# Performance work log

Measured on AMD Instinct MI355X. Metric: run time of the kernel, lower is better.

The kernel has to match this reference:

```python
import jax, jax.numpy as jnp
import numpy as np

N = 100000
E = 600000
G = 8
HID = 128
HEADS = 4
C = HID // HEADS  # 32


def setup_inputs() -> dict:
    key = jax.random.key(0)
    ks = jax.random.split(key, 32)
    s = 0.05
    node_numeric = jax.random.normal(ks[0], (N, 8), jnp.float32)
    node_cat0 = jax.random.randint(ks[1], (N,), 0, 32)
    node_cat1 = jax.random.randint(ks[2], (N,), 0, 64)
    edge_numeric = jax.random.normal(ks[3], (E, 4), jnp.float32)
    edge_cat0 = jax.random.randint(ks[4], (E,), 0, 16)
    edge_cat1 = jax.random.randint(ks[5], (E,), 0, 100)
    src = jax.random.randint(ks[6], (E,), 0, N)
    dst = jax.random.randint(ks[7], (E,), 0, N)
    dst = jnp.where(dst == src, (dst + 1) % N, dst)  # GATConv removes self-loops before adding its own
    edge_index = jnp.stack([src, dst])
    batch = jnp.sort(jax.random.randint(ks[8], (N,), 0, G))
    recipe = jax.random.normal(ks[9], (G, 16), jnp.float32)
    return dict(
        node_numeric=node_numeric, node_cat0=node_cat0, node_cat1=node_cat1,
        edge_numeric=edge_numeric, edge_cat0=edge_cat0, edge_cat1=edge_cat1,
        edge_index=edge_index, batch=batch, recipe=recipe,
        emb_node0=jax.random.normal(ks[10], (32, 6), jnp.float32) * s,
        emb_node1=jax.random.normal(ks[11], (64, 8), jnp.float32) * s,
        emb_edge0=jax.random.normal(ks[12], (16, 4), jnp.float32) * s,
        emb_edge1=jax.random.normal(ks[13], (100, 10), jnp.float32) * s,
        W_in=jax.random.normal(ks[14], (38, HID), jnp.float32) * s,
        b_in=jnp.zeros((HID,), jnp.float32),
        W_edge=jax.random.normal(ks[15], (18, HID), jnp.float32) * s,
        b_edge=jnp.zeros((HID,), jnp.float32),
        gat_lin=jax.random.normal(ks[16], (3, HID, HID), jnp.float32) * s,
        gat_lin_edge=jax.random.normal(ks[17], (3, HID, HID), jnp.float32) * s,
        att_src=jax.random.normal(ks[18], (3, HEADS, C), jnp.float32) * s,
        att_dst=jax.random.normal(ks[19], (3, HEADS, C), jnp.float32) * s,
        att_edge=jax.random.normal(ks[20], (3, HEADS, C), jnp.float32) * s,
        gat_bias=jnp.zeros((3, HID), jnp.float32),
        W_r1=jax.random.normal(ks[21], (HID, HID), jnp.float32) * s,
        b_r1=jnp.zeros((HID,), jnp.float32),
        W_r2=jax.random.normal(ks[22], (HID, 1), jnp.float32) * s,
        b_r2=jnp.zeros((1,), jnp.float32),
    )


def _segment_softmax(logits, seg, num):
    m = jax.ops.segment_max(logits, seg, num_segments=num)
    ex = jnp.exp(logits - m[seg])
    s = jax.ops.segment_sum(ex, seg, num_segments=num)
    return ex / s[seg]


def _forward(node_numeric, edge_numeric, recipe,
             emb_node0, emb_node1, emb_edge0, emb_edge1,
             W_in, b_in, W_edge, b_edge,
             gat_lin, gat_lin_edge, att_src, att_dst, att_edge, gat_bias,
             W_r1, b_r1, W_r2, b_r2,
             node_cat0, node_cat1, edge_cat0, edge_cat1, edge_index, batch):
    n = node_numeric.shape[0]
    src, dst = edge_index[0], edge_index[1]
    # node encoding: numeric + categorical embeddings + broadcast recipe
    h = jnp.concatenate([node_numeric, emb_node0[node_cat0], emb_node1[node_cat1], recipe[batch]], axis=1)
    h = jax.nn.relu(h @ W_in + b_in)
    # edge encoding (shared across GAT layers)
    e = jnp.concatenate([edge_numeric, emb_edge0[edge_cat0], emb_edge1[edge_cat1]], axis=1)
    e = e @ W_edge + b_edge
    # self-loops with fill_value='mean': per-dst mean of incoming edge_attr
    cnt = jax.ops.segment_sum(jnp.ones((e.shape[0],), e.dtype), dst, num_segments=n)
    loop = jax.ops.segment_sum(e, dst, num_segments=n) / jnp.maximum(cnt, 1.0)[:, None]
    ar = jnp.arange(n)
    src_a = jnp.concatenate([src, ar])
    dst_a = jnp.concatenate([dst, ar])
    e_a = jnp.concatenate([e, loop], axis=0)  # [E+N, HID]
    for l in range(gat_lin.shape[0]):
        x = (h @ gat_lin[l]).reshape(n, HEADS, C)          # shared lin_src/lin_dst
        ee = (e_a @ gat_lin_edge[l]).reshape(-1, HEADS, C)
        a_s = jnp.sum(x * att_src[l], axis=-1)   # [N, HEADS]
        a_d = jnp.sum(x * att_dst[l], axis=-1)
        a_e = jnp.sum(ee * att_edge[l], axis=-1)  # [E+N, HEADS]
        logits = jax.nn.leaky_relu(a_s[src_a] + a_d[dst_a] + a_e, negative_slope=0.2)
        alpha = _segment_softmax(logits, dst_a, n)  # segment softmax over dst
        out = jax.ops.segment_sum(x[src_a] * alpha[:, :, None], dst_a, num_segments=n)
        h = jax.nn.relu(out.reshape(n, HID) + gat_bias[l])  # dropout off (eval)
    g = jax.ops.segment_sum(h, batch, num_segments=G)  # global_add_pool
    g = jax.nn.relu(g @ W_r1 + b_r1)
    return g @ W_r2 + b_r2  # [G, 1]


def reference(node_numeric, node_cat0, node_cat1, edge_numeric, edge_cat0, edge_cat1,
              edge_index, batch, recipe,
              emb_node0, emb_node1, emb_edge0, emb_edge1,
              W_in, b_in, W_edge, b_edge,
              gat_lin, gat_lin_edge, att_src, att_dst, att_edge, gat_bias,
              W_r1, b_r1, W_r2, b_r2):
    return _forward(node_numeric, edge_numeric, recipe,
                    emb_node0, emb_node1, emb_edge0, emb_edge1,
                    W_in, b_in, W_edge, b_edge,
                    gat_lin, gat_lin_edge, att_src, att_dst, att_edge, gat_bias,
                    W_r1, b_r1, W_r2, b_r2,
                    node_cat0, node_cat1, edge_cat0, edge_cat1, edge_index, batch)
```

## Files before the change

### kernel.cpp

```cpp
#include <hip/hip_runtime.h>
#include <math.h>

#define HID 128

typedef float f32x4 __attribute__((ext_vector_type(4)));
typedef short bf16x8 __attribute__((ext_vector_type(8)));
typedef unsigned int uint32;

__device__ __forceinline__ float leaky02(float z) { return z >= 0.f ? z : 0.2f * z; }
__device__ __forceinline__ unsigned short f2bf(float f) {
  uint32 u = __float_as_uint(f);
  u = (u + 0x7fff + ((u >> 16) & 1)) >> 16;
  return (unsigned short)u;
}
__device__ __forceinline__ float bf2f(uint32 us) { return __uint_as_float(us << 16); }
__device__ __forceinline__ float bflo(uint32 w) { return __uint_as_float(w << 16); }
__device__ __forceinline__ float bfhi(uint32 w) { return __uint_as_float(w & 0xffff0000u); }

__global__ void k_enc(const float* __restrict__ nodenum, const int* __restrict__ c0,
                      const int* __restrict__ c1, const int* __restrict__ batch,
                      const float* __restrict__ recipe,
                      const float* __restrict__ e0, const float* __restrict__ e1,
                      const float* __restrict__ Win, const float* __restrict__ bin,
                      unsigned short* __restrict__ hb, int n) {
  __shared__ float f[8][40];
  __shared__ int idx[8][3];
  int t = threadIdx.x;
  int col = t & 127;
  int half = t >> 7;
  float w[40];
#pragma unroll
  for (int k = 0; k < 38; k++) w[k] = Win[k * 128 + col];
  w[38] = 0.f;
  w[39] = 0.f;
  float bias = bin[col];
  int ntiles = (n + 7) / 8;
  for (int tile = blockIdx.x; tile < ntiles; tile += gridDim.x) {
    int base = tile * 8;
    if (t < 64) {
      int r = t >> 3, k = t & 7;
      int v = base + r;
      f[r][k] = (v < n) ? nodenum[(size_t)v * 8 + k] : 0.f;
    } else if (t < 88) {
      int j = t - 64;
      int r = j / 3, which = j - r * 3;
      int v = base + r;
      int val = 0;
      if (v < n) val = (which == 0) ? c0[v] : ((which == 1) ? c1[v] : batch[v]);
      idx[r][which] = val;
    } else if (t >= 240) {
      int r = t - 240;
      if (r < 8) { f[r][38] = 0.f; f[r][39] = 0.f; }
    }
    __syncthreads();
    if (t < 240) {
      int r = t / 30, k = t - r * 30;
      float val;
      if (k < 6) val = e0[idx[r][0] * 6 + k];
      else if (k < 14) val = e1[idx[r][1] * 8 + (k - 6)];
      else val = recipe[idx[r][2] * 16 + (k - 14)];
      f[r][8 + k] = val;
    }
    __syncthreads();
#pragma unroll
    for (int rr = 0; rr < 4; rr++) {
      int r = half * 4 + rr;
      int v = base + r;
      float acc = bias;
#pragma unroll
      for (int k4 = 0; k4 < 10; k4++) {
        float4 fv = *(const float4*)(&f[r][k4 * 4]);
        acc += fv.x * w[k4 * 4] + fv.y * w[k4 * 4 + 1] + fv.z * w[k4 * 4 + 2] +
               fv.w * w[k4 * 4 + 3];
      }
      if (v < n) hb[(size_t)v * 128 + col] = f2bf(fmaxf(acc, 0.f));
    }
    __syncthreads();
  }
}

__global__ void k_prep(const float* __restrict__ gle, const float* __restrict__ atte,
                       const float* __restrict__ We, const float* __restrict__ be,
                       float* __restrict__ P, float* __restrict__ q) {
  __shared__ float M[512];
  int l = blockIdx.x;
  int t = threadIdx.x;
#pragma unroll
  for (int i = 0; i < 2; i++) {
    int idx = t + i * 256;
    int k = idx >> 2, hh = idx & 3;
    float acc = 0.f;
    for (int c = 0; c < 32; c++)
      acc += gle[l * 16384 + k * 128 + hh * 32 + c] * atte[l * 128 + hh * 32 + c];
    M[k * 4 + hh] = acc;
  }
  __syncthreads();
  if (t < 72) {
    int j = t >> 2, hh = t & 3;
    float acc = 0.f;
    for (int k = 0; k < 128; k++) acc += We[j * 128 + k] * M[k * 4 + hh];
    P[(l * 18 + j) * 4 + hh] = acc;
  } else if (t < 76) {
    int hh = t - 72;
    float acc = 0.f;
    for (int k = 0; k < 128; k++) acc += be[k] * M[k * 4 + hh];
    q[l * 4 + hh] = acc;
  }
}

__global__ void k_wprep(const float* __restrict__ glin, unsigned short* __restrict__ WbfT) {
  int idx = blockIdx.x * 256 + threadIdx.x;
  if (idx >= 3 * 128 * 128) return;
  int l = idx >> 14;
  int rem = idx & 16383;
  int col = rem >> 7;
  int k = rem & 127;
  WbfT[idx] = f2bf(glin[(l << 14) + k * 128 + col]);
}

__global__ void k_deg(const int* __restrict__ dst, int* __restrict__ cnt, int E) {
  int i = blockIdx.x * 256 + threadIdx.x;
  if (i < E) atomicAdd(&cnt[dst[i]], 1);
}

__global__ void k_ae(const float* __restrict__ enum_, const int* __restrict__ ec0,
                     const int* __restrict__ ec1, const int* __restrict__ dst,
                     const int* __restrict__ srcarr,
                     const float* __restrict__ ee0, const float* __restrict__ ee1,
                     const float* __restrict__ P, const float* __restrict__ q,
                     int* __restrict__ cursor, float* __restrict__ ae3,
                     int* __restrict__ srcc, int E) {
  __shared__ float Ps[216];
  __shared__ float qs[12];
  int t = threadIdx.x;
  for (int i = t; i < 216; i += 256) Ps[i] = P[i];
  if (t < 12) qs[t] = q[t];
  __syncthreads();
  int i = blockIdx.x * 256 + t;
  if (i >= E) return;
  float raw[18];
  float4 nm = *(const float4*)(enum_ + (size_t)i * 4);
  raw[0] = nm.x; raw[1] = nm.y; raw[2] = nm.z; raw[3] = nm.w;
  int a0 = ec0[i], a1 = ec1[i];
  float4 eb0 = *(const float4*)(ee0 + a0 * 4);
  raw[4] = eb0.x; raw[5] = eb0.y; raw[6] = eb0.z; raw[7] = eb0.w;
#pragma unroll
  for (int j = 0; j < 10; j++) raw[8 + j] = ee1[a1 * 10 + j];
  int d = dst[i];
  int pos = atomicAdd(&cursor[d], 1);
  srcc[pos] = srcarr[i];
#pragma unroll
  for (int l = 0; l < 3; l++) {
    float o[4];
#pragma unroll
    for (int hh = 0; hh < 4; hh++) {
      float acc = qs[l * 4 + hh];
#pragma unroll
      for (int j = 0; j < 18; j++) acc += raw[j] * Ps[(l * 18 + j) * 4 + hh];
      o[hh] = acc;
    }
    *(float4*)(ae3 + ((size_t)l * E + pos) * 4) = make_float4(o[0], o[1], o[2], o[3]);
  }
}

__global__ void k_loopmean(const float* __restrict__ ae3, const int* __restrict__ rowptr,
                           float* __restrict__ aeL, int n, int E) {
  int v = blockIdx.x * 256 + threadIdx.x;
  if (v >= n) return;
  int beg = rowptr[v], end = rowptr[v + 1];
  float inv = (end > beg) ? 1.f / (float)(end - beg) : 0.f;
#pragma unroll
  for (int l = 0; l < 3; l++) {
    float4 s = make_float4(0.f, 0.f, 0.f, 0.f);
    const float4* base = (const float4*)(ae3 + (size_t)l * E * 4);
    for (int j = beg; j < end; j++) {
      float4 a = base[j];
      s.x += a.x; s.y += a.y; s.z += a.z; s.w += a.w;
    }
    *(float4*)(aeL + ((size_t)l * n + v) * 4) =
        make_float4(s.x * inv, s.y * inv, s.z * inv, s.w * inv);
  }
}

__global__ void k_scan1(const int* __restrict__ cnt, int* __restrict__ excl,
                        int* __restrict__ bsum, int n) {
  __shared__ int sh[256];
  int t = threadIdx.x;
  int i = blockIdx.x * 256 + t;
  int v = (i < n) ? cnt[i] : 0;
  sh[t] = v;
  __syncthreads();
  for (int off = 1; off < 256; off <<= 1) {
    int add = (t >= off) ? sh[t - off] : 0;
    __syncthreads();
    sh[t] += add;
    __syncthreads();
  }
  if (i < n) excl[i] = sh[t] - v;
  if (t == 255) bsum[blockIdx.x] = sh[255];
}

__global__ void k_scan2(int* __restrict__ bsum, int nb) {
  __shared__ int sh[512];
  int t = threadIdx.x;
  int v = (t < nb) ? bsum[t] : 0;
  sh[t] = v;
  __syncthreads();
  for (int off = 1; off < 512; off <<= 1) {
    int add = (t >= off) ? sh[t - off] : 0;
    __syncthreads();
    sh[t] += add;
    __syncthreads();
  }
  if (t < nb) bsum[t] = sh[t] - v;
}

__global__ void k_scan3(int* __restrict__ rowptr, const int* __restrict__ boff,
                        int* __restrict__ cursor, int n, int E) {
  int i = blockIdx.x * 256 + threadIdx.x;
  if (i < n) {
    int val = rowptr[i] + boff[i >> 8];
    rowptr[i] = val;
    cursor[i] = val;
  }
  if (i == 0) rowptr[n] = E;
}

__global__ void __launch_bounds__(512, 4)
k_x(const unsigned short* __restrict__ hb, const unsigned short* __restrict__ WbfT,
    const float* __restrict__ att_s, const float* __restrict__ att_d,
    unsigned short* __restrict__ xb, float* __restrict__ a_s,
    float* __restrict__ a_d, int n) {
  __shared__ unsigned short hs[64 * 128];
  int t = threadIdx.x;
  int w = t >> 6, l = t & 63;
  int ch = w >> 2, wr = w & 3;
  int lr = l & 15, lg = l >> 4;
  bf16x8 bfrag[4][4];
#pragma unroll
  for (int ct = 0; ct < 4; ct++) {
#pragma unroll
    for (int ks = 0; ks < 4; ks++) {
      int col = ch * 64 + ct * 16 + lr;
      int k0 = ks * 32 + lg * 8;
      bfrag[ct][ks] = *(const bf16x8*)(WbfT + col * 128 + k0);
    }
  }
  float avs[4], avd[4];
#pragma unroll
  for (int ct = 0; ct < 4; ct++) {
    avs[ct] = att_s[ch * 64 + ct * 16 + lr];
    avd[ct] = att_d[ch * 64 + ct * 16 + lr];
  }
  for (int tb = blockIdx.x * 64; tb < n; tb += gridDim.x * 64) {
    __syncthreads();
#pragma unroll
    for (int i = 0; i < 2; i++) {
      int idx = t + i * 512;
      int r = idx >> 4, c = idx & 15;
      uint4 vv = make_uint4(0, 0, 0, 0);
      if (tb + r < n) vv = *(const uint4*)(hb + (size_t)(tb + r) * 128 + c * 8);
      *(uint4*)(&hs[r * 128 + ((c ^ (r & 7)) * 8)]) = vv;
    }
    __syncthreads();
    f32x4 acc[4];
#pragma unroll
    for (int ct = 0; ct < 4; ct++) acc[ct] = (f32x4){0.f, 0.f, 0.f, 0.f};
#pragma unroll
    for (int ks = 0; ks < 4; ks++) {
      int r = wr * 16 + lr;
      int c = ks * 4 + lg;
      bf16x8 a = *(const bf16x8*)(&hs[r * 128 + ((c ^ (r & 7)) * 8)]);
#pragma unroll
      for (int ct = 0; ct < 4; ct++)
        acc[ct] = __builtin_amdgcn_mfma_f32_16x16x32_bf16(a, bfrag[ct][ks], acc[ct], 0, 0, 0);
    }
#pragma unroll
    for (int j = 0; j < 4; j++) {
      int row = tb + wr * 16 + lg * 4 + j;
      bool ok = row < n;
      if (ok) {
#pragma unroll
        for (int ct = 0; ct < 4; ct++)
          xb[(size_t)row * 128 + ch * 64 + ct * 16 + lr] = f2bf(acc[ct][j]);
      }
      float psA = acc[0][j] * avs[0] + acc[1][j] * avs[1];
      float pdA = acc[0][j] * avd[0] + acc[1][j] * avd[1];
      float psB = acc[2][j] * avs[2] + acc[3][j] * avs[3];
      float pdB = acc[2][j] * avd[2] + acc[3][j] * avd[3];
#pragma unroll
      for (int m = 1; m <= 8; m <<= 1) {
        psA += __shfl_xor(psA, m); pdA += __shfl_xor(pdA, m);
        psB += __shfl_xor(psB, m); pdB += __shfl_xor(pdB, m);
      }
      if (lr == 0 && ok) {
        a_s[(size_t)row * 4 + ch * 2] = psA;
        a_s[(size_t)row * 4 + ch * 2 + 1] = psB;
        a_d[(size_t)row * 4 + ch * 2] = pdA;
        a_d[(size_t)row * 4 + ch * 2 + 1] = pdB;
      }
    }
  }
}

__global__ void k_agg(const unsigned short* __restrict__ xb, const float* __restrict__ a_s,
                      const float* __restrict__ a_d, const float* __restrict__ ae3,
                      const float* __restrict__ aeL,
                      const int* __restrict__ rowptr, const int* __restrict__ srcc,
                      const float* __restrict__ bias,
                      unsigned short* __restrict__ hbout, int n, int E, int l) {
  int wid = threadIdx.x >> 6;
  int v = blockIdx.x * 4 + wid;
  if (v >= n) return;
  int lane = threadIdx.x & 63;
  int el = lane >> 2;
  int hh = lane & 3;
  float ad_own = a_d[(size_t)v * 4 + hh];
  float as_own = a_s[(size_t)v * 4 + hh];
  float aeL_own = aeL[((size_t)l * n + v) * 4 + hh];
  float m_own = leaky02(as_own + ad_own + aeL_own);
  float s_own = 1.f;
  int c2 = lane * 2;
  int headO = lane >> 4;
  const char* xB = (const char*)xb;
  uint32 coff = (uint32)c2 * 2u;
  uint32 wv = *(const uint32*)(xB + ((uint32)v << 8) + coff);
  float a0 = bflo(wv);
  float a1 = bfhi(wv);
  int beg = rowptr[v], end = rowptr[v + 1];
  const float* aeB = ae3 + (size_t)l * E * 4;
  for (int cb = beg; cb < end; cb += 16) {
    int ne = end - cb;
    if (ne > 16) ne = 16;
    float logit = -1e30f;
    int srcE = 0;
    if (el < ne) {
      int j = cb + el;
      srcE = srcc[j];
      float asrc = a_s[(size_t)srcE * 4 + hh];
      float aev = aeB[(size_t)j * 4 + hh];
      logit = leaky02(asrc + ad_own + aev);
    }
    float cm = logit;
    cm = fmaxf(cm, __shfl_xor(cm, 4));
    cm = fmaxf(cm, __shfl_xor(cm, 8));
    cm = fmaxf(cm, __shfl_xor(cm, 16));
    cm = fmaxf(cm, __shfl_xor(cm, 32));
    float mn_own = fmaxf(m_own, cm);
    float p = (el < ne) ? __expf(logit - mn_own) : 0.f;
    float ps = p;
    ps += __shfl_xor(ps, 4);
    ps += __shfl_xor(ps, 8);
    ps += __shfl_xor(ps, 16);
    ps += __shfl_xor(ps, 32);
    float c_own = __expf(m_own - mn_own);
    m_own = mn_own;
    s_own = s_own * c_own + ps;
    float cO = __shfl(c_own, headO);
    a0 *= cO;
    a1 *= cO;
    int e = 0;
    for (; e + 2 <= ne; e += 2) {
      int se0 = __builtin_amdgcn_readlane(srcE, e * 4);
      int se1 = __builtin_amdgcn_readlane(srcE, e * 4 + 4);
      float p0 = __shfl(p, e * 4 + headO);
      float p1 = __shfl(p, e * 4 + 4 + headO);
      uint32 x0 = *(const uint32*)(xB + ((uint32)se0 << 8) + coff);
      uint32 x1 = *(const uint32*)(xB + ((uint32)se1 << 8) + coff);
      a0 += p0 * bflo(x0) + p1 * bflo(x1);
      a1 += p0 * bfhi(x0) + p1 * bfhi(x1);
    }
    if (e < ne) {
      int se = __builtin_amdgcn_readlane(srcE, e * 4);
      float pC = __shfl(p, e * 4 + headO);
      uint32 xw = *(const uint32*)(xB + ((uint32)se << 8) + coff);
      a0 += pC * bflo(xw);
      a1 += pC * bfhi(xw);
    }
  }
  float sO = __shfl(s_own, headO);
  float r0 = fmaxf(a0 / sO + bias[l * HID + c2], 0.f);
  float r1 = fmaxf(a1 / sO + bias[l * HID + c2 + 1], 0.f);
  uint32 pk = (uint32)f2bf(r0) | ((uint32)f2bf(r1) << 16);
  *(uint32*)(hbout + (size_t)v * HID + c2) = pk;
}

__global__ void k_pool(const unsigned short* __restrict__ hb, const int* __restrict__ batch,
                       float* __restrict__ g, int n) {
  int t = threadIdx.x;
  int per = (n + gridDim.x - 1) / gridDim.x;
  int start = blockIdx.x * per;
  int end = min(n, start + per);
  float acc = 0.f;
  int cur = -1;
  for (int v = start; v < end; v++) {
    int b = batch[v];
    if (b != cur) {
      if (cur >= 0) atomicAdd(&g[cur * 128 + t], acc);
      acc = 0.f;
      cur = b;
    }
    acc += bf2f((uint32)hb[(size_t)v * 128 + t]);
  }
  if (cur >= 0) atomicAdd(&g[cur * 128 + t], acc);
}

__global__ void k_head(const float* __restrict__ g, const float* __restrict__ Wr1,
                       const float* __restrict__ br1, const float* __restrict__ Wr2,
                       const float* __restrict__ br2, float* __restrict__ out, int G_) {
  __shared__ float gl[128];
  __shared__ float red[128];
  int i = blockIdx.x;
  int t = threadIdx.x;
  gl[t] = g[i * 128 + t];
  __syncthreads();
  float acc = br1[t];
  for (int k = 0; k < 128; k++) acc += gl[k] * Wr1[k * 128 + t];
  float hv = fmaxf(acc, 0.f);
  red[t] = hv * Wr2[t];
  __syncthreads();
  for (int off = 64; off >= 1; off >>= 1) {
    if (t < off) red[t] += red[t + off];
    __syncthreads();
  }
  if (t == 0) out[i] = red[0] + br2[0];
}

extern "C" void kernel_launch(void* const* d_in, const int* in_sizes, int n_in,
                              void* d_out, int out_size, void* d_ws, size_t ws_size,
                              hipStream_t stream) {
  const float* node_numeric = (const float*)d_in[0];
  const int* node_cat0 = (const int*)d_in[1];
  const int* node_cat1 = (const int*)d_in[2];
  const float* edge_numeric = (const float*)d_in[3];
  const int* edge_cat0 = (const int*)d_in[4];
  const int* edge_cat1 = (const int*)d_in[5];
  const int* edge_index = (const int*)d_in[6];
  const int* batch = (const int*)d_in[7];
  const float* recipe = (const float*)d_in[8];
  const float* emb_node0 = (const float*)d_in[9];
  const float* emb_node1 = (const float*)d_in[10];
  const float* emb_edge0 = (const float*)d_in[11];
  const float* emb_edge1 = (const float*)d_in[12];
  const float* W_in = (const float*)d_in[13];
  const float* b_in = (const float*)d_in[14];
  const float* W_edge = (const float*)d_in[15];
  const float* b_edge = (const float*)d_in[16];
  const float* gat_lin = (const float*)d_in[17];
  const float* gat_lin_edge = (const float*)d_in[18];
  const float* att_src = (const float*)d_in[19];
  const float* att_dst = (const float*)d_in[20];
  const float* att_edge = (const float*)d_in[21];
  const float* gat_bias = (const float*)d_in[22];
  const float* W_r1 = (const float*)d_in[23];
  const float* b_r1 = (const float*)d_in[24];
  const float* W_r2 = (const float*)d_in[25];
  const float* b_r2 = (const float*)d_in[26];

  int N = in_sizes[0] / 8;
  int E = in_sizes[3] / 4;
  int Gn = in_sizes[8] / 16;
  const int* srcArr = edge_index;
  const int* dstArr = edge_index + E;

  char* ws = (char*)d_ws;
  size_t o = 0;
  auto alloc = [&](size_t b) {
    char* p = ws + o;
    o = (o + b + 255) & ~(size_t)255;
    return p;
  };
  unsigned short* hbf = (unsigned short*)alloc((size_t)N * 128 * 2);
  unsigned short* xbf = (unsigned short*)alloc((size_t)N * 128 * 2);
  float* ae3 = (float*)alloc((size_t)E * 12 * 4);
  float* aeL = (float*)alloc((size_t)N * 12 * 4);
  float* a_s = (float*)alloc((size_t)N * 4 * 4);
  float* a_d = (float*)alloc((size_t)N * 4 * 4);
  float* P = (float*)alloc(216 * 4);
  float* q = (float*)alloc(12 * 4);
  unsigned short* WbfT = (unsigned short*)alloc(3 * 128 * 128 * 2);
  int* cnt = (int*)alloc((size_t)N * 4);
  int* rowptr = (int*)alloc((size_t)(N + 1) * 4);
  int* cursor = (int*)alloc((size_t)N * 4);
  int* bsum = (int*)alloc(512 * 4);
  int* srcc = (int*)alloc((size_t)E * 4);
  float* g = (float*)alloc((size_t)Gn * 128 * 4);
  (void)ws_size;

  (void)hipMemsetAsync(cnt, 0, (size_t)N * 4, stream);
  (void)hipMemsetAsync(g, 0, (size_t)Gn * 128 * 4, stream);

  int nbl = (N + 255) / 256;
  int ebl = (E + 255) / 256;

  k_enc<<<2048, 256, 0, stream>>>(node_numeric, node_cat0, node_cat1, batch, recipe,
                                  emb_node0, emb_node1, W_in, b_in, hbf, N);
  k_prep<<<3, 256, 0, stream>>>(gat_lin_edge, att_edge, W_edge, b_edge, P, q);
  k_wprep<<<192, 256, 0, stream>>>(gat_lin, WbfT);
  k_deg<<<ebl, 256, 0, stream>>>(dstArr, cnt, E);
  k_scan1<<<nbl, 256, 0, stream>>>(cnt, rowptr, bsum, N);
  k_scan2<<<1, 512, 0, stream>>>(bsum, nbl);
  k_scan3<<<nbl, 256, 0, stream>>>(rowptr, bsum, cursor, N, E);
  k_ae<<<ebl, 256, 0, stream>>>(edge_numeric, edge_cat0, edge_cat1, dstArr, srcArr,
                                emb_edge0, emb_edge1, P, q, cursor, ae3, srcc, E);
  k_loopmean<<<nbl, 256, 0, stream>>>(ae3, rowptr, aeL, N, E);

  for (int l = 0; l < 3; l++) {
    k_x<<<1024, 512, 0, stream>>>(hbf, WbfT + l * 16384, att_src + l * 128,
                                  att_dst + l * 128, xbf, a_s, a_d, N);
    k_agg<<<(N + 3) / 4, 256, 0, stream>>>(xbf, a_s, a_d, ae3, aeL, rowptr, srcc,
                                           gat_bias, hbf, N, E, l);
  }
  k_pool<<<1024, 128, 0, stream>>>(hbf, batch, g, N);
  k_head<<<Gn, 128, 0, stream>>>(g, W_r1, b_r1, W_r2, b_r2, (float*)d_out, Gn);
}
```

Measured before the change: 435.4 us.

## Split attention-score computation out of node GEMM and load A-fragments directly

The node linear kernel no longer stages input rows through shared memory with barriers. Each wave now loads its MFMA A-fragments straight from global memory, and the per-head attention dot products are removed from it. A new kernel, launched after the GEMM, reads the bf16 outputs back and computes a_s and a_d with wave shuffles. This removes LDS traffic, barriers and epilogue reductions from the GEMM, at the cost of an extra launch and a reread of the node feature matrix per layer. The attention scores are now computed from bf16-rounded values instead of fp32 accumulators, which slightly changes the numerics.

```diff
diff --git a/kernel.cpp b/kernel.cpp
--- a/kernel.cpp
+++ b/kernel.cpp
@@ -228,10 +228,7 @@
 
 __global__ void __launch_bounds__(512, 4)
 k_x(const unsigned short* __restrict__ hb, const unsigned short* __restrict__ WbfT,
-    const float* __restrict__ att_s, const float* __restrict__ att_d,
-    unsigned short* __restrict__ xb, float* __restrict__ a_s,
-    float* __restrict__ a_d, int n) {
-  __shared__ unsigned short hs[64 * 128];
+    unsigned short* __restrict__ xb, int n) {
   int t = threadIdx.x;
   int w = t >> 6, l = t & 63;
   int ch = w >> 2, wr = w & 3;
@@ -246,59 +243,52 @@
       bfrag[ct][ks] = *(const bf16x8*)(WbfT + col * 128 + k0);
     }
   }
-  float avs[4], avd[4];
-#pragma unroll
-  for (int ct = 0; ct < 4; ct++) {
-    avs[ct] = att_s[ch * 64 + ct * 16 + lr];
-    avd[ct] = att_d[ch * 64 + ct * 16 + lr];
-  }
-  for (int tb = blockIdx.x * 64; tb < n; tb += gridDim.x * 64) {
-    __syncthreads();
-#pragma unroll
-    for (int i = 0; i < 2; i++) {
-      int idx = t + i * 512;
-      int r = idx >> 4, c = idx & 15;
-      uint4 vv = make_uint4(0, 0, 0, 0);
-      if (tb + r < n) vv = *(const uint4*)(hb + (size_t)(tb + r) * 128 + c * 8);
-      *(uint4*)(&hs[r * 128 + ((c ^ (r & 7)) * 8)]) = vv;
-    }
-    __syncthreads();
+  int ntiles = (n + 63) >> 6;
+  for (int tile = blockIdx.x; tile < ntiles; tile += gridDim.x) {
+    int rowA = tile * 64 + wr * 16 + lr;
+    int rowL = min(rowA, n - 1);
     f32x4 acc[4];
 #pragma unroll
     for (int ct = 0; ct < 4; ct++) acc[ct] = (f32x4){0.f, 0.f, 0.f, 0.f};
 #pragma unroll
     for (int ks = 0; ks < 4; ks++) {
-      int r = wr * 16 + lr;
-      int c = ks * 4 + lg;
-      bf16x8 a = *(const bf16x8*)(&hs[r * 128 + ((c ^ (r & 7)) * 8)]);
+      bf16x8 a = *(const bf16x8*)(hb + (size_t)rowL * 128 + ks * 32 + lg * 8);
 #pragma unroll
       for (int ct = 0; ct < 4; ct++)
         acc[ct] = __builtin_amdgcn_mfma_f32_16x16x32_bf16(a, bfrag[ct][ks], acc[ct], 0, 0, 0);
     }
 #pragma unroll
     for (int j = 0; j < 4; j++) {
-      int row = tb + wr * 16 + lg * 4 + j;
-      bool ok = row < n;
-      if (ok) {
+      int row = tile * 64 + wr * 16 + lg * 4 + j;
+      if (row < n) {
 #pragma unroll
         for (int ct = 0; ct < 4; ct++)
           xb[(size_t)row * 128 + ch * 64 + ct * 16 + lr] = f2bf(acc[ct][j]);
       }
-      float psA = acc[0][j] * avs[0] + acc[1][j] * avs[1];
-      float pdA = acc[0][j] * avd[0] + acc[1][j] * avd[1];
-      float psB = acc[2][j] * avs[2] + acc[3][j] * avs[3];
-      float pdB = acc[2][j] * avd[2] + acc[3][j] * avd[3];
-#pragma unroll
-      for (int m = 1; m <= 8; m <<= 1) {
-        psA += __shfl_xor(psA, m); pdA += __shfl_xor(pdA, m);
-        psB += __shfl_xor(psB, m); pdB += __shfl_xor(pdB, m);
-      }
-      if (lr == 0 && ok) {
-        a_s[(size_t)row * 4 + ch * 2] = psA;
-        a_s[(size_t)row * 4 + ch * 2 + 1] = psB;
-        a_d[(size_t)row * 4 + ch * 2] = pdA;
-        a_d[(size_t)row * 4 + ch * 2 + 1] = pdB;
-      }
+    }
+  }
+}
+
+__global__ void k_att(const unsigned short* __restrict__ xb, const float* __restrict__ att_s,
+                      const float* __restrict__ att_d, float* __restrict__ a_s,
+                      float* __restrict__ a_d, int n) {
+  int t = threadIdx.x;
+  int wid = t >> 6, lane = t & 63;
+  int head = lane >> 4;
+  float as0 = att_s[lane * 2], as1 = att_s[lane * 2 + 1];
+  float ad0 = att_d[lane * 2], ad1 = att_d[lane * 2 + 1];
+  for (int v = blockIdx.x * 4 + wid; v < n; v += gridDim.x * 4) {
+    uint32 xw = *(const uint32*)(xb + (size_t)v * 128 + lane * 2);
+    float x0 = bflo(xw), x1 = bfhi(xw);
+    float ps = x0 * as0 + x1 * as1;
+    float pd = x0 * ad0 + x1 * ad1;
+    ps += __shfl_xor(ps, 1); pd += __shfl_xor(pd, 1);
+    ps += __shfl_xor(ps, 2); pd += __shfl_xor(pd, 2);
+    ps += __shfl_xor(ps, 4); pd += __shfl_xor(pd, 4);
+    ps += __shfl_xor(ps, 8); pd += __shfl_xor(pd, 8);
+    if ((lane & 15) == 0) {
+      a_s[(size_t)v * 4 + head] = ps;
+      a_d[(size_t)v * 4 + head] = pd;
     }
   }
 }
@@ -506,8 +496,9 @@
   k_loopmean<<<nbl, 256, 0, stream>>>(ae3, rowptr, aeL, N, E);
 
   for (int l = 0; l < 3; l++) {
-    k_x<<<1024, 512, 0, stream>>>(hbf, WbfT + l * 16384, att_src + l * 128,
-                                  att_dst + l * 128, xbf, a_s, a_d, N);
+    k_x<<<1024, 512, 0, stream>>>(hbf, WbfT + l * 16384, xbf, N);
+    k_att<<<2048, 256, 0, stream>>>(xbf, att_src + l * 128, att_dst + l * 128,
+                                    a_s, a_d, N);
     k_agg<<<(N + 3) / 4, 256, 0, stream>>>(xbf, a_s, a_d, ae3, aeL, rowptr, srcc,
                                            gat_bias, hbf, N, E, l);
   }
```

Result: slower. 464.2 us (+6.6%).
